# Performance work log

Measured on AMD Instinct MI355X. Metric: run time of the kernel, lower is better.

Reference implementation:

```python
import jax, jax.numpy as jnp
import numpy as np

H, W, C = 768, 768, 64


def _segment_ids(mask):
    """mask: [L] int binary separator mask -> [L] int32 segment ids.
    A new grid segment starts at each rising edge (0 -> 1) of the mask;
    pixel 0 always belongs to segment 0. Equivalent to GridStructureBuilder's
    run-based row/column partition, derived via a single cumsum."""
    m = mask.astype(jnp.int32)
    prev = jnp.concatenate([jnp.zeros((1,), jnp.int32), m[:-1]])
    rising = ((m == 1) & (prev == 0)).at[0].set(False)
    return jnp.cumsum(rising.astype(jnp.int32))


def setup_inputs() -> dict:
    key = jax.random.key(0)
    k1, k2, k3 = jax.random.split(key, 3)
    return {
        "input": jax.random.normal(k1, (1, H, W, C), dtype=jnp.float32),
        "h_mask": jax.random.randint(k2, (1, H), 0, 2, dtype=jnp.int32),
        "v_mask": jax.random.randint(k3, (1, W), 0, 2, dtype=jnp.int32),
    }


def reference(input, h_mask, v_mask):
    x = input[0]                      # [H, W, C]
    h, w, c = x.shape
    row_ids = _segment_ids(h_mask[0])  # [H]
    col_ids = _segment_ids(v_mask[0])  # [W]
    # flat cell id per pixel; w is a static upper bound on the column count
    idx = (row_ids[:, None] * w + col_ids[None, :]).reshape(-1)  # [H*W]
    xf = x.reshape(h * w, c)
    n_seg = h * w                      # static upper bound on cell count
    sums = jax.ops.segment_sum(xf, idx, num_segments=n_seg)           # [n_seg, C]
    counts = jax.ops.segment_sum(jnp.ones((h * w,), x.dtype), idx,
                                 num_segments=n_seg)                  # [n_seg]
    # scatter-add of (1/area)*x == per-cell mean
    means = sums / jnp.maximum(counts, 1.0)[:, None]
    # keep_size=True: gather cell means back to every pixel
    return means[idx].reshape(1, h, w, c)
```

## Files before the change

### kernel.cpp

```cpp
#include <hip/hip_runtime.h>


#define GH 768
#define GW 768
#define GC 64
#define MAXSEG 385

enum {
    OFF_ROWSTART = 0,
    OFF_ROWEND   = OFF_ROWSTART + MAXSEG,
    OFF_COLSTART = OFF_ROWEND + MAXSEG,
    OFF_COLEND   = OFF_COLSTART + MAXSEG,
    OFF_NROWS    = OFF_COLEND + MAXSEG,
    OFF_NCOLS    = OFF_NROWS + 1,
};

__global__ __launch_bounds__(768) void seg_scan(const int* __restrict__ h_mask,
                                                const int* __restrict__ v_mask,
                                                int* __restrict__ ws) {
    __shared__ int s[GH];
    const int i = threadIdx.x;
    const bool is_row = (blockIdx.x == 0);
    const int* m = is_row ? h_mask : v_mask;

    int mi = m[i];
    int rising = 0;
    if (i > 0) rising = (mi == 1 && m[i - 1] == 0) ? 1 : 0;
    s[i] = rising;
    __syncthreads();

    for (int off = 1; off < GH; off <<= 1) {
        int add = (i >= off) ? s[i - off] : 0;
        __syncthreads();
        s[i] += add;
        __syncthreads();
    }

    const int seg  = s[i];
    const int segL = (i == 0)      ? -1 : s[i - 1];
    const int segR = (i == GH - 1) ? -2 : s[i + 1];

    int* start = ws + (is_row ? OFF_ROWSTART : OFF_COLSTART);
    int* end   = ws + (is_row ? OFF_ROWEND   : OFF_COLEND);
    if (seg != segL) start[seg] = i;
    if (seg != segR) end[seg]   = i + 1;
    if (i == GH - 1) ws[is_row ? OFF_NROWS : OFF_NCOLS] = seg + 1;
}

__global__ __launch_bounds__(256) void cell_pool(const float4* __restrict__ in,
                                                 float4* __restrict__ out,
                                                 const int* __restrict__ ws) {
    const int nrows  = ws[OFF_NROWS];
    const int ncols  = ws[OFF_NCOLS];
    const int ncells = nrows * ncols;

    const int wave   = blockIdx.x * 4 + (threadIdx.x >> 6);
    const int nwaves = gridDim.x * 4;
    const int lane   = threadIdx.x & 63;
    const int pg     = lane >> 4;
    const int cq     = lane & 15;

    for (int cell = wave; cell < ncells; cell += nwaves) {
        const int br = cell / ncols;
        const int bc = cell - br * ncols;
        const int y0 = ws[OFF_ROWSTART + br];
        const int y1 = ws[OFF_ROWEND + br];
        const int x0 = ws[OFF_COLSTART + bc];
        const int x1 = ws[OFF_COLEND + bc];

        float4 acc = make_float4(0.f, 0.f, 0.f, 0.f);
        for (int y = y0; y < y1; ++y) {
            const size_t rb = (size_t)(y * GW) * 16 + cq;
            for (int x = x0 + pg; x < x1; x += 4) {
                float4 v = in[rb + (size_t)x * 16];
                acc.x += v.x; acc.y += v.y; acc.z += v.z; acc.w += v.w;
            }
        }
        #pragma unroll
        for (int msk = 16; msk < 64; msk <<= 1) {
            acc.x += __shfl_xor(acc.x, msk, 64);
            acc.y += __shfl_xor(acc.y, msk, 64);
            acc.z += __shfl_xor(acc.z, msk, 64);
            acc.w += __shfl_xor(acc.w, msk, 64);
        }
        const float area = (float)((y1 - y0) * (x1 - x0));
        float4 mean;
        mean.x = acc.x / area; mean.y = acc.y / area;
        mean.z = acc.z / area; mean.w = acc.w / area;

        for (int y = y0; y < y1; ++y) {
            const size_t rb = (size_t)(y * GW) * 16 + cq;
            for (int x = x0 + pg; x < x1; x += 4) {
                out[rb + (size_t)x * 16] = mean;
            }
        }
    }
}

extern "C" void kernel_launch(void* const* d_in, const int* in_sizes, int n_in,
                              void* d_out, int out_size, void* d_ws, size_t ws_size,
                              hipStream_t stream) {
    const float* in  = (const float*)d_in[0];
    const int* hmask = (const int*)d_in[1];
    const int* vmask = (const int*)d_in[2];
    float* out = (float*)d_out;
    int* ws = (int*)d_ws;

    seg_scan<<<2, GH, 0, stream>>>(hmask, vmask, ws);
    cell_pool<<<2048, 256, 0, stream>>>((const float4*)in, (float4*)out, ws);
}
```

Baseline: 281.5 us.

## Split pooling into compact cell-mean pass and coalesced per-pixel broadcast

The cell-mean kernel now walks each cell's pixels as a flat sequence, so all four pixel groups of a wave stay busy even for narrow cells. It writes one mean per cell instead of writing it back to every pixel in place. A separate grid-stride kernel then fills the output linearly, looking up each pixel's row and column segment ids. This is meant to replace the poorly coalesced per-cell output stores with fully contiguous writes, at the cost of an extra launch and an intermediate means buffer in the workspace. If the workspace is too small, a fallback path stores the mean at each cell's anchor pixel and broadcasts from there.

New measurement: 283.8 us. No clear change (+0.8%).

```diff
diff --git a/kernel.cpp b/kernel.cpp
--- a/kernel.cpp
+++ b/kernel.cpp
@@ -3,7 +3,6 @@
 
 #define GH 768
 #define GW 768
-#define GC 64
 #define MAXSEG 385
 
 enum {
@@ -13,6 +12,9 @@
     OFF_COLEND   = OFF_COLSTART + MAXSEG,
     OFF_NROWS    = OFF_COLEND + MAXSEG,
     OFF_NCOLS    = OFF_NROWS + 1,
+    OFF_ROWID    = OFF_NCOLS + 1,
+    OFF_COLID    = OFF_ROWID + GH,
+    OFF_MEANS    = 4096,
 };
 
 __global__ __launch_bounds__(768) void seg_scan(const int* __restrict__ h_mask,
@@ -40,6 +42,8 @@
     const int segL = (i == 0)      ? -1 : s[i - 1];
     const int segR = (i == GH - 1) ? -2 : s[i + 1];
 
+    ws[(is_row ? OFF_ROWID : OFF_COLID) + i] = seg;
+
     int* start = ws + (is_row ? OFF_ROWSTART : OFF_COLSTART);
     int* end   = ws + (is_row ? OFF_ROWEND   : OFF_COLEND);
     if (seg != segL) start[seg] = i;
@@ -47,9 +51,10 @@
     if (i == GH - 1) ws[is_row ? OFF_NROWS : OFF_NCOLS] = seg + 1;
 }
 
-__global__ __launch_bounds__(256) void cell_pool(const float4* __restrict__ in,
-                                                 float4* __restrict__ out,
-                                                 const int* __restrict__ ws) {
+__global__ __launch_bounds__(256) void cell_mean(const float4* __restrict__ in,
+                                                 float4* __restrict__ dst,
+                                                 const int* __restrict__ ws,
+                                                 int anchor_mode) {
     const int nrows  = ws[OFF_NROWS];
     const int ncols  = ws[OFF_NCOLS];
     const int ncells = nrows * ncols;
@@ -67,15 +72,45 @@
         const int y1 = ws[OFF_ROWEND + br];
         const int x0 = ws[OFF_COLSTART + bc];
         const int x1 = ws[OFF_COLEND + bc];
+        const int w   = x1 - x0;
+        const int npx = w * (y1 - y0);
+        const int q16 = 16 / w;
+        const int r16 = 16 - q16 * w;
 
-        float4 acc = make_float4(0.f, 0.f, 0.f, 0.f);
-        for (int y = y0; y < y1; ++y) {
-            const size_t rb = (size_t)(y * GW) * 16 + cq;
-            for (int x = x0 + pg; x < x1; x += 4) {
-                float4 v = in[rb + (size_t)x * 16];
-                acc.x += v.x; acc.y += v.y; acc.z += v.z; acc.w += v.w;
+        int wy[4], wx[4];
+        #pragma unroll
+        for (int k = 0; k < 4; ++k) {
+            int t  = x0 + pg + 4 * k;
+            int yy = y0;
+            while (t >= x1) { t -= w; ++yy; }
+            wx[k] = t; wy[k] = yy;
+        }
+
+        float4 a0 = make_float4(0.f, 0.f, 0.f, 0.f);
+        float4 a1 = a0, a2 = a0, a3 = a0;
+
+        const int nit = (npx + 15) >> 4;
+        for (int it = 0; it < nit; ++it) {
+            if (wy[0] < y1) { float4 v = in[(wy[0] * GW + wx[0]) * 16 + cq];
+                a0.x += v.x; a0.y += v.y; a0.z += v.z; a0.w += v.w; }
+            if (wy[1] < y1) { float4 v = in[(wy[1] * GW + wx[1]) * 16 + cq];
+                a1.x += v.x; a1.y += v.y; a1.z += v.z; a1.w += v.w; }
+            if (wy[2] < y1) { float4 v = in[(wy[2] * GW + wx[2]) * 16 + cq];
+                a2.x += v.x; a2.y += v.y; a2.z += v.z; a2.w += v.w; }
+            if (wy[3] < y1) { float4 v = in[(wy[3] * GW + wx[3]) * 16 + cq];
+                a3.x += v.x; a3.y += v.y; a3.z += v.z; a3.w += v.w; }
+            #pragma unroll
+            for (int k = 0; k < 4; ++k) {
+                wx[k] += r16; wy[k] += q16;
+                if (wx[k] >= x1) { wx[k] -= w; wy[k] += 1; }
             }
         }
+
+        float4 acc;
+        acc.x = (a0.x + a1.x) + (a2.x + a3.x);
+        acc.y = (a0.y + a1.y) + (a2.y + a3.y);
+        acc.z = (a0.z + a1.z) + (a2.z + a3.z);
+        acc.w = (a0.w + a1.w) + (a2.w + a3.w);
         #pragma unroll
         for (int msk = 16; msk < 64; msk <<= 1) {
             acc.x += __shfl_xor(acc.x, msk, 64);
@@ -83,17 +118,48 @@
             acc.z += __shfl_xor(acc.z, msk, 64);
             acc.w += __shfl_xor(acc.w, msk, 64);
         }
-        const float area = (float)((y1 - y0) * (x1 - x0));
-        float4 mean;
-        mean.x = acc.x / area; mean.y = acc.y / area;
-        mean.z = acc.z / area; mean.w = acc.w / area;
 
-        for (int y = y0; y < y1; ++y) {
-            const size_t rb = (size_t)(y * GW) * 16 + cq;
-            for (int x = x0 + pg; x < x1; x += 4) {
-                out[rb + (size_t)x * 16] = mean;
-            }
+        if (lane < 16) {
+            const float inv = 1.f / (float)npx;
+            float4 mean = make_float4(acc.x * inv, acc.y * inv,
+                                      acc.z * inv, acc.w * inv);
+            const int oidx = anchor_mode ? (y0 * GW + x0) * 16 + lane
+                                         : cell * 16 + lane;
+            dst[oidx] = mean;
         }
+    }
+}
+
+__global__ __launch_bounds__(256) void bcast_ws(float4* __restrict__ out,
+                                                const float4* __restrict__ means,
+                                                const int* __restrict__ ws) {
+    const int ncols = ws[OFF_NCOLS];
+    int g = blockIdx.x * 256 + threadIdx.x;
+    #pragma unroll 3
+    for (int it = 0; it < 18; ++it, g += 2048 * 256) {
+        const int p  = g >> 4;
+        const int cq = g & 15;
+        const int y  = p / GW;
+        const int x  = p - y * GW;
+        const int rid = ws[OFF_ROWID + y];
+        const int cid = ws[OFF_COLID + x];
+        out[g] = means[(rid * ncols + cid) * 16 + cq];
+    }
+}
+
+__global__ __launch_bounds__(256) void bcast_anchor(float4* out,
+                                                    const int* __restrict__ ws) {
+    int g = blockIdx.x * 256 + threadIdx.x;
+    for (int it = 0; it < 18; ++it, g += 2048 * 256) {
+        const int p  = g >> 4;
+        const int cq = g & 15;
+        const int y  = p / GW;
+        const int x  = p - y * GW;
+        const int rid = ws[OFF_ROWID + y];
+        const int cid = ws[OFF_COLID + x];
+        const int ya  = ws[OFF_ROWSTART + rid];
+        const int xa  = ws[OFF_COLSTART + cid];
+        out[g] = out[(ya * GW + xa) * 16 + cq];
     }
 }
 
@@ -107,5 +173,15 @@
     int* ws = (int*)d_ws;
 
     seg_scan<<<2, GH, 0, stream>>>(hmask, vmask, ws);
-    cell_pool<<<2048, 256, 0, stream>>>((const float4*)in, (float4*)out, ws);
+
+    const size_t need = (size_t)OFF_MEANS * 4
+                      + (size_t)MAXSEG * MAXSEG * 64 * 4;
+    if (ws_size >= need) {
+        float4* means = (float4*)(ws + OFF_MEANS);
+        cell_mean<<<2048, 256, 0, stream>>>((const float4*)in, means, ws, 0);
+        bcast_ws<<<2048, 256, 0, stream>>>((float4*)out, means, ws);
+    } else {
+        cell_mean<<<2048, 256, 0, stream>>>((const float4*)in, (float4*)out, ws, 1);
+        bcast_anchor<<<2048, 256, 0, stream>>>((float4*)out, ws);
+    }
 }
```
